# Kernel optimization log

Hardware: AMD Instinct MI355X
Metric: run time of the kernel (lower is better)

Reference implementation:

```python
import jax, jax.numpy as jnp
import numpy as np

NEG_SLOPE = 0.2

def gat_layer(x, src, dst, W, a_src, a_dst, num_nodes):
    """PyG-style GATConv. W:[F_in,H*C], a_src/a_dst:[H,C]. Returns [N,H,C]."""
    H, C = a_src.shape
    h = (x @ W).reshape(num_nodes, H, C)                      # [N,H,C]
    e_src = jnp.sum(h * a_src, axis=-1)                       # [N,H]
    e_dst = jnp.sum(h * a_dst, axis=-1)                       # [N,H]
    e = jax.nn.leaky_relu(e_src[src] + e_dst[dst], NEG_SLOPE) # [E,H]
    # segment softmax over incoming edges of each destination node
    m = jax.ops.segment_max(e, dst, num_segments=num_nodes)
    w = jnp.exp(e - m[dst])
    z = jax.ops.segment_sum(w, dst, num_segments=num_nodes)
    alpha = w / (z[dst] + 1e-16)                               # [E,H]
    msg = h[src] * alpha[:, :, None]                           # [E,H,C]
    return jax.ops.segment_sum(msg, dst, num_segments=num_nodes)


def setup_inputs() -> dict:
    key = jax.random.key(0)
    ks = jax.random.split(key, 16)
    N, E, F_IN, HID, A, G = 50000, 800000, 128, 128, 32, 64
    x = jax.random.normal(ks[0], (N, F_IN), dtype=jnp.float32)
    edge_index = jax.random.randint(ks[1], (2, E), 0, N, dtype=jnp.int32)
    batch = jnp.sort(jax.random.randint(ks[2], (N,), 0, G, dtype=jnp.int32))
    s = 0.1
    W1 = jax.random.normal(ks[3], (F_IN, 2 * HID), jnp.float32) * s
    a_src1 = jax.random.normal(ks[4], (2, HID), jnp.float32) * s
    a_dst1 = jax.random.normal(ks[5], (2, HID), jnp.float32) * s
    b1 = jnp.zeros((2 * HID,), jnp.float32)
    W2 = jax.random.normal(ks[6], (2 * HID, HID), jnp.float32) * s
    a_src2 = jax.random.normal(ks[7], (1, HID), jnp.float32) * s
    a_dst2 = jax.random.normal(ks[8], (1, HID), jnp.float32) * s
    b2 = jnp.zeros((HID,), jnp.float32)
    Wp = jax.random.normal(ks[9], (HID, A), jnp.float32) * s
    bp = jnp.zeros((A,), jnp.float32)
    Wv = jax.random.normal(ks[10], (HID, 1), jnp.float32) * s
    bv = jnp.zeros((1,), jnp.float32)
    return {"x": x, "edge_index": edge_index, "batch": batch,
            "W1": W1, "a_src1": a_src1, "a_dst1": a_dst1, "b1": b1,
            "W2": W2, "a_src2": a_src2, "a_dst2": a_dst2, "b2": b2,
            "Wp": Wp, "bp": bp, "Wv": Wv, "bv": bv}


def reference(x, edge_index, batch, W1, a_src1, a_dst1, b1,
              W2, a_src2, a_dst2, b2, Wp, bp, Wv, bv):
    N = x.shape[0]
    G = 64  # number of graphs in the batch
    # add self-loops (PyG GATConv default)
    loop = jnp.arange(N, dtype=edge_index.dtype)
    src = jnp.concatenate([edge_index[0], loop])
    dst = jnp.concatenate([edge_index[1], loop])
    # layer 1: heads=2, concat=True
    h1 = gat_layer(x, src, dst, W1, a_src1, a_dst1, N)        # [N,2,HID]
    h1 = jax.nn.elu(h1.reshape(N, -1) + b1)                   # [N,2*HID]
    # layer 2: heads=1, concat=False (mean over heads = identity for H=1)
    h2 = gat_layer(h1, src, dst, W2, a_src2, a_dst2, N)       # [N,1,HID]
    h2 = jax.nn.elu(h2.reshape(N, -1) + b2)                   # [N,HID]
    # global mean pool over graphs
    sums = jax.ops.segment_sum(h2, batch, num_segments=G)
    cnt = jax.ops.segment_sum(jnp.ones((N,), h2.dtype), batch, num_segments=G)
    x_pool = sums / jnp.maximum(cnt, 1.0)[:, None]            # [G,HID]
    policy_logits = x_pool @ Wp + bp                          # [G,A]
    state_value = x_pool @ Wv + bv                            # [G,1]
    return (policy_logits, state_value)
```

## Files before the change

kernel.cpp:

```cpp
#include <hip/hip_runtime.h>
#include <hip/hip_bf16.h>
#include <cstdint>


typedef __attribute__((ext_vector_type(8))) short bf16x8;
typedef __attribute__((ext_vector_type(4))) float f32x4;

#define NBLK_H 160
#define BSH 6
#define BMSK 63

__device__ __forceinline__ float wave_sum(float v) {
#pragma unroll
    for (int off = 32; off >= 1; off >>= 1) v += __shfl_xor(v, off, 64);
    return v;
}

__device__ __forceinline__ unsigned short f2bf(float f) {
    union { float f; uint32_t u; } c; c.f = f;
    uint32_t u = c.u;
    return (unsigned short)((u + 0x7fffu + ((u >> 16) & 1u)) >> 16);
}

__device__ __forceinline__ float bf2f(unsigned short u) {
    union { uint32_t u; float f; } c; c.u = ((uint32_t)u) << 16;
// ... 13 lines not shown
    int cg_ = rest;
    int quad = lane >> 4, lo = lane & 15;
    int col = colOff + cg_ * CPW + c * 16 + lo;
    unsigned short v[8];
#pragma unroll
    for (int j = 0; j < 8; ++j)
        v[j] = f2bf(W[(t * 32 + quad * 8 + j) * ldW + col]);
    ushort4* dst = (ushort4*)(Bsw + (size_t)tid * 8);
    ushort4 o0, o1;
    o0.x = v[0]; o0.y = v[1]; o0.z = v[2]; o0.w = v[3];
    o1.x = v[4]; o1.y = v[5]; o1.z = v[6]; o1.w = v[7];
    dst[0] = o0; dst[1] = o1;
}


__global__ __launch_bounds__(256) void init_kernel(
        const float* __restrict__ W1, const float* __restrict__ W2,
        const float* __restrict__ a_src1, const float* __restrict__ a_dst1,
        unsigned short* __restrict__ B1h0, unsigned short* __restrict__ B1h1,
        unsigned short* __restrict__ B2,
        float* __restrict__ v1s, float* __restrict__ v1d,
        int* __restrict__ zbase, int zn4, int ZB,
        const int* __restrict__ ei, int* __restrict__ hist,
        int E, int ET, int CHUNK, int NB) {
    __shared__ int bins[1024];
    int b = blockIdx.x;
    if (b < 8)        swizzle_body<128, 128>(W1, 256, 0,   B1h0, b * 256 + threadIdx.x);
    else if (b < 16)  swizzle_body<128, 128>(W1, 256, 128, B1h1, (b - 8) * 256 + threadIdx.x);
    else if (b < 32)  swizzle_body<256, 128>(W2, 128, 0,   B2, (b - 16) * 256 + threadIdx.x);
    else if (b == 32) {
        int t = threadIdx.x, h = t >> 7, k = t & 127;
        float vs = 0.f, vd = 0.f;
        for (int c = 0; c < 128; ++c) {
            float w = W1[k * 256 + h * 128 + c];
            vs += w * a_src1[h * 128 + c];
            vd += w * a_dst1[h * 128 + c];
        }
        v1s[h * 128 + k] = vs;
        v1d[h * 128 + k] = vd;
    } else if (b < 33 + ZB) {
        int i = (b - 33) * 256 + threadIdx.x;
        if (i < zn4) ((int4*)zbase)[i] = make_int4(0, 0, 0, 0);
    } else {
        const int blk = b - 33 - ZB;
        for (int t = threadIdx.x; t < NB; t += 256) bins[t] = 0;
        __syncthreads();
        const int start = blk * CHUNK, end = min(ET, start + CHUNK);
        for (int i = start + threadIdx.x; i < end; i += 256) {
            int dst = (i < E) ? ei[E + i] : (i - E);
            atomicAdd(&bins[dst >> BSH], 1);
        }
        __syncthreads();
        for (int t = threadIdx.x; t < NB; t += 256) hist[t * NBLK_H + blk] = bins[t];
    }
}


__global__ __launch_bounds__(256) void scan_attn1(
        int* __restrict__ hist, int* __restrict__ tsum, int M, int TILESH,
        const float* __restrict__ x, const float* __restrict__ v1s,
        const float* __restrict__ v1d, float* __restrict__ es1,
        float* __restrict__ ed1, unsigned short* __restrict__ xbf, int N) {
    __shared__ int buf[256];
    if ((int)blockIdx.x < TILESH) {
        const int t = threadIdx.x;
        const int base = blockIdx.x * 1024 + t * 4;
        int v[4]; int s = 0;
#pragma unroll
        for (int k = 0; k < 4; ++k) { v[k] = (base + k < M) ? hist[base + k] : 0; s += v[k]; }
        buf[t] = s;
        __syncthreads();
#pragma unroll
        for (int off = 1; off < 256; off <<= 1) {
            int xx = (t >= off) ? buf[t - off] : 0;
            __syncthreads();
            buf[t] += xx;
            __syncthreads();
        }
        int run = buf[t] - s;
#pragma unroll
        for (int k = 0; k < 4; ++k) {
            if (base + k < M) hist[base + k] = run;
            run += v[k];
        }
        if (t == 255) tsum[blockIdx.x] = buf[255];
        return;
    }
    int bid = blockIdx.x - TILESH;
    int wid = (bid * 256 + threadIdx.x) >> 6;
    int lane = threadIdx.x & 63;
    if (wid >= N) return;
    float2 xv = *(const float2*)(x + (size_t)wid * 128 + lane * 2);
    float p0s = xv.x * v1s[lane * 2] + xv.y * v1s[lane * 2 + 1];
    float p1s = xv.x * v1s[128 + lane * 2] + xv.y * v1s[128 + lane * 2 + 1];
    float p0d = xv.x * v1d[lane * 2] + xv.y * v1d[lane * 2 + 1];
    float p1d = xv.x * v1d[128 + lane * 2] + xv.y * v1d[128 + lane * 2 + 1];
    p0s = wave_sum(p0s); p1s = wave_sum(p1s);
    p0d = wave_sum(p0d); p1d = wave_sum(p1d);
    if (lane == 0) {
        es1[wid * 2] = p0s; es1[wid * 2 + 1] = p1s;
        ed1[wid * 2] = p0d; ed1[wid * 2 + 1] = p1d;
    }
    ushort2 o; o.x = f2bf(xv.x); o.y = f2bf(xv.y);
    *(ushort2*)(xbf + (size_t)wid * 128 + lane * 2) = o;
}


__global__ __launch_bounds__(256) void part_kernel(const int* __restrict__ ei,
                                                   const int* __restrict__ hist,
                                                   const int* __restrict__ tsum,
                                                   int* __restrict__ bsorted,
                                                   int* __restrict__ segbase,
                                                   int E, int ET, int CHUNK, int NB, int T) {
    __shared__ int sb[256];
    __shared__ int scur[1024];
    const int t = threadIdx.x;
    sb[t] = (t < T) ? tsum[t] : 0;
    __syncthreads();
#pragma unroll
    for (int off = 1; off < 256; off <<= 1) {
        int v = (t >= off) ? sb[t - off] : 0;
        __syncthreads();
        sb[t] += v;
        __syncthreads();
    }
    const int blk = blockIdx.x;
    for (int b = t; b < NB; b += 256) {
        int idx = b * NBLK_H + blk;
        int tile = idx >> 10;
        int v = hist[idx] + (tile ? sb[tile - 1] : 0);
        scur[b] = v;
        if (blk == 0) segbase[b] = v;
    }
    if (blk == 0 && t == 0) segbase[NB] = sb[T - 1];
    __syncthreads();
    const int start = blk * CHUNK, end = min(ET, start + CHUNK);
    for (int i = start + t; i < end; i += 256) {
        int dst = (i < E) ? ei[E + i] : (i - E);
        int src = (i < E) ? ei[i] : dst;
        int pos = atomicAdd(&scur[dst >> BSH], 1);
        bsorted[pos] = (src << BSH) | (dst & BMSK);
    }
}


__global__ __launch_bounds__(256) void bucket_kernel(const int* __restrict__ bsorted,
                                                     const int* __restrict__ segbase,
                                                     const float* __restrict__ es1,
                                                     const float* __restrict__ ed1,
                                                     int* __restrict__ csr_src,
                                                     float2* __restrict__ csr_alpha,
                                                     int* __restrict__ rowptr,
                                                     int N, int NB) {
    __shared__ int cnt[64], excl[64];
    __shared__ float z0[64], z1[64];
    __shared__ float2 edv[64];
    __shared__ int ebuf[3072];
    __shared__ float2 wbuf[3072];
    const int b = blockIdx.x;
    const int gbase = segbase[b], gend = segbase[b + 1];
    const int sz = gend - gbase;
    const int t = threadIdx.x;
    if (b == 0 && t == 0) rowptr[N] = segbase[NB];
    if (t < 64) {
        cnt[t] = 0; z0[t] = 0.f; z1[t] = 0.f;
        int dst = (b << BSH) + t;
        if (dst < N) edv[t] = *(const float2*)(ed1 + dst * 2);
        else edv[t] = make_float2(0.f, 0.f);
    }
    __syncthreads();
    const bool fits = (sz <= 3072);
    for (int i = t; i < sz; i += 256) {
        int p = bsorted[gbase + i];
        int s = p >> BSH, ld = p & BMSK;
        float2 esv = *(const float2*)(es1 + s * 2);
        float e0 = esv.x + edv[ld].x; e0 = (e0 > 0.f) ? e0 : 0.2f * e0;
        float e1 = esv.y + edv[ld].y; e1 = (e1 > 0.f) ? e1 : 0.2f * e1;
        float w0 = __expf(e0), w1 = __expf(e1);
        if (fits) { ebuf[i] = p; wbuf[i] = make_float2(w0, w1); }
        atomicAdd(&z0[ld], w0);
        atomicAdd(&z1[ld], w1);
        atomicAdd(&cnt[ld], 1);
    }
    __syncthreads();
    if (t < 64) excl[t] = cnt[t];
    __syncthreads();
    for (int off = 1; off < 64; off <<= 1) {
        int v = (t < 64 && t >= off) ? excl[t - off] : 0;
        __syncthreads();
        if (t < 64) excl[t] += v;
        __syncthreads();
    }
    if (t < 64) {
        int dst = (b << BSH) + t;
        if (dst < N) rowptr[dst] = gbase + excl[t] - cnt[t];
    }
    __syncthreads();
    if (t < 64) {
        cnt[t] = excl[t] - cnt[t];
        z0[t] = 1.f / (z0[t] + 1e-16f);
        z1[t] = 1.f / (z1[t] + 1e-16f);
    }
    __syncthreads();
    if (fits) {
        for (int i = t; i < sz; i += 256) {
            int p = ebuf[i]; float2 wv = wbuf[i];
            int ld = p & BMSK;
            int pos = atomicAdd(&cnt[ld], 1);
            csr_src[gbase + pos] = p >> BSH;
            csr_alpha[gbase + pos] = make_float2(wv.x * z0[ld], wv.y * z1[ld]);
        }
    } else {
        for (int i = t; i < sz; i += 256) {
            int p = bsorted[gbase + i];
            int s = p >> BSH, ld = p & BMSK;
            float2 esv = *(const float2*)(es1 + s * 2);
            float e0 = esv.x + edv[ld].x; e0 = (e0 > 0.f) ? e0 : 0.2f * e0;
            float e1 = esv.y + edv[ld].y; e1 = (e1 > 0.f) ? e1 : 0.2f * e1;
            float w0 = __expf(e0), w1 = __expf(e1);
            int pos = atomicAdd(&cnt[ld], 1);
            csr_src[gbase + pos] = s;
            csr_alpha[gbase + pos] = make_float2(w0 * z0[ld], w1 * z1[ld]);
        }
    }
}


#define ACC2(U_, WW_, P_, Q_) { float v_;                              \
    v_ = bf2f(U_.x); P_.x += WW_.x * v_; Q_.x += WW_.y * v_;           \
    v_ = bf2f(U_.y); P_.y += WW_.x * v_; Q_.y += WW_.y * v_;           \
    v_ = bf2f(U_.z); P_.z += WW_.x * v_; Q_.z += WW_.y * v_;           \
    v_ = bf2f(U_.w); P_.w += WW_.x * v_; Q_.w += WW_.y * v_; }

__global__ void gat_agg_x(const unsigned short* __restrict__ xbf,
                          const int* __restrict__ rowptr, const int* __restrict__ csr_src,
                          const float2* __restrict__ csr_alpha,
                          unsigned short* __restrict__ aggx, int N, int NPAD) {
// ... 178 lines not shown
            }
        }
    }
    __syncthreads();
    if (tid < 64) {
        int row = tid;
        int n = n0 + row;
        if (n < N) {
            es[n] = lds_ps[0][row] + lds_ps[1][row] + lds_ps[2][row] + lds_ps[3][row];
            ed[n] = lds_pd[0][row] + lds_pd[1][row] + lds_pd[2][row] + lds_pd[3][row];
        }
    }
}


__global__ void alpha2_kernel(const int* __restrict__ rowptr, const int* __restrict__ csr_src,
                              const float* __restrict__ es, const float* __restrict__ ed,
                              float* __restrict__ csr_a2, int N) {
    int wid = (blockIdx.x * blockDim.x + threadIdx.x) >> 6;
    int lane = threadIdx.x & 63;
    if (wid >= N) return;
    const int rs = rowptr[wid], re = rowptr[wid + 1];
    const float edn = ed[wid];
    float z = 0.f;
    for (int i = rs; i < re; i += 64) {
        int cnt = min(re - i, 64);
        if (lane < cnt) {
            int s = csr_src[i + lane];
            float e = es[s] + edn;
            e = (e > 0.f) ? e : 0.2f * e;
            float w = __expf(e);
            csr_a2[i + lane] = w;
            z += w;
        }
    }
    z = wave_sum(z);
    const float rz = 1.f / (z + 1e-16f);
    for (int i = rs + lane; i < re; i += 64) csr_a2[i] *= rz;
}


#define ACC1(U_, W_, P_) {                                   \
    P_.x += W_ * bf2f(U_.x); P_.y += W_ * bf2f(U_.y);        \
    P_.z += W_ * bf2f(U_.z); P_.w += W_ * bf2f(U_.w); }

__global__ void gat_agg_h1(const unsigned short* __restrict__ Hpre,
                           const int* __restrict__ rowptr, const int* __restrict__ csr_src,
                           const float* __restrict__ csr_a2,
                           const float* __restrict__ bias, unsigned short* __restrict__ out,
                           int N) {
    __shared__ int   s_lds[4][2][32];
    __shared__ float a_lds[4][2][32];
    const int wave = threadIdx.x >> 6, lane = threadIdx.x & 63;
    const int g = lane >> 5, c = lane & 31;
    const int node = (blockIdx.x * 4 + wave) * 2 + g;
    if (node >= N) return;
    const int rs = rowptr[node], re = rowptr[node + 1];
    float4 p = {0.f, 0.f, 0.f, 0.f};
    for (int i = rs; i < re; i += 32) {
        const int cnt = min(re - i, 32);
        if (c < cnt) {
            s_lds[wave][g][c] = csr_src[i + c];
            a_lds[wave][g][c] = csr_a2[i + c];
        }
        int k = 0;
        for (; k + 7 < cnt; k += 8) {
            int s0 = s_lds[wave][g][k + 0], s1 = s_lds[wave][g][k + 1];
            int s2 = s_lds[wave][g][k + 2], s3 = s_lds[wave][g][k + 3];
            int s4 = s_lds[wave][g][k + 4], s5 = s_lds[wave][g][k + 5];
            int s6 = s_lds[wave][g][k + 6], s7 = s_lds[wave][g][k + 7];
            float a0 = a_lds[wave][g][k + 0], a1 = a_lds[wave][g][k + 1];
            float a2 = a_lds[wave][g][k + 2], a3 = a_lds[wave][g][k + 3];
            float a4 = a_lds[wave][g][k + 4], a5 = a_lds[wave][g][k + 5];
            float a6 = a_lds[wave][g][k + 6], a7 = a_lds[wave][g][k + 7];
            ushort4 u0 = *(const ushort4*)(Hpre + (size_t)s0 * 128 + c * 4);
            ushort4 u1 = *(const ushort4*)(Hpre + (size_t)s1 * 128 + c * 4);
            ushort4 u2 = *(const ushort4*)(Hpre + (size_t)s2 * 128 + c * 4);
            ushort4 u3 = *(const ushort4*)(Hpre + (size_t)s3 * 128 + c * 4);
            ushort4 u4 = *(const ushort4*)(Hpre + (size_t)s4 * 128 + c * 4);
            ushort4 u5 = *(const ushort4*)(Hpre + (size_t)s5 * 128 + c * 4);
            ushort4 u6 = *(const ushort4*)(Hpre + (size_t)s6 * 128 + c * 4);
            ushort4 u7 = *(const ushort4*)(Hpre + (size_t)s7 * 128 + c * 4);
            ACC1(u0, a0, p);
            ACC1(u1, a1, p);
            ACC1(u2, a2, p);
            ACC1(u3, a3, p);
            ACC1(u4, a4, p);
            ACC1(u5, a5, p);
            ACC1(u6, a6, p);
            ACC1(u7, a7, p);
        }
        for (; k < cnt; ++k) {
            int s0 = s_lds[wave][g][k];
            float a0 = a_lds[wave][g][k];
            ushort4 u0 = *(const ushort4*)(Hpre + (size_t)s0 * 128 + c * 4);
            ACC1(u0, a0, p);
        }
    }
    float4 bv = ((const float4*)bias)[c];
    float ox = p.x + bv.x, oy = p.y + bv.y, oz = p.z + bv.z, ow = p.w + bv.w;
    ox = (ox > 0.f) ? ox : __expf(ox) - 1.f;
    oy = (oy > 0.f) ? oy : __expf(oy) - 1.f;
    oz = (oz > 0.f) ? oz : __expf(oz) - 1.f;
    ow = (ow > 0.f) ? ow : __expf(ow) - 1.f;
    ushort4 o;
    o.x = f2bf(ox); o.y = f2bf(oy); o.z = f2bf(oz); o.w = f2bf(ow);
    *(ushort4*)(out + (size_t)node * 128 + c * 4) = o;
}


#define PCHUNK 256

__global__ __launch_bounds__(256) void pool_partial(const unsigned short* __restrict__ h2,
                                                    const int* __restrict__ batch,
                                                    float* __restrict__ xsum,
                                                    int* __restrict__ cnt, int N) {
    const int base = blockIdx.x * PCHUNK;
    const int rg = threadIdx.x >> 6;
    const int c2 = threadIdx.x & 63;
    float ax = 0.f, ay = 0.f;
    int gcur = -1, run = 0;
    for (int r = rg; r < PCHUNK; r += 4) {
        int i = base + r;
        if (i >= N) break;
        int g = batch[i];
        if (g != gcur) {
            if (gcur >= 0) {
                atomicAdd(&xsum[gcur * 128 + c2 * 2 + 0], ax);
                atomicAdd(&xsum[gcur * 128 + c2 * 2 + 1], ay);
                if (c2 == 0) atomicAdd(&cnt[gcur], run);
            }
            gcur = g; ax = 0.f; ay = 0.f; run = 0;
        }
        ushort2 u = *(const ushort2*)(h2 + (size_t)i * 128 + c2 * 2);
        ax += bf2f(u.x); ay += bf2f(u.y);
        run += 1;
    }
    if (gcur >= 0) {
        atomicAdd(&xsum[gcur * 128 + c2 * 2 + 0], ax);
        atomicAdd(&xsum[gcur * 128 + c2 * 2 + 1], ay);
        if (c2 == 0) atomicAdd(&cnt[gcur], run);
    }
}


__global__ void head_kernel(const float* __restrict__ xsum, const int* __restrict__ cnt,
                            const float* __restrict__ Wp, const float* __restrict__ bp,
                            const float* __restrict__ Wv, const float* __restrict__ bv,
                            float* __restrict__ out) {
    int g = blockIdx.x, t = threadIdx.x;
    __shared__ float p[128];
    float inv = 1.f / fmaxf((float)cnt[g], 1.f);
    p[t] = xsum[g * 128 + t] * inv;
    p[t + 64] = xsum[g * 128 + t + 64] * inv;
    __syncthreads();
    if (t < 32) {
        float acc = bp[t];
        for (int k = 0; k < 128; ++k) acc += p[k] * Wp[k * 32 + t];
        out[g * 32 + t] = acc;
    } else if (t == 32) {
        float acc = bv[0];
        for (int k = 0; k < 128; ++k) acc += p[k] * Wv[k];
        out[64 * 32 + g] = acc;
    }
}


extern "C" void kernel_launch(void* const* d_in, const int* in_sizes, int n_in,
                              void* d_out, int out_size, void* d_ws, size_t ws_size,
                              hipStream_t stream) {
    const float* x      = (const float*)d_in[0];
    const int*   ei     = (const int*)d_in[1];
    const int*   batch  = (const int*)d_in[2];
    const float* W1     = (const float*)d_in[3];
    const float* a_src1 = (const float*)d_in[4];
    const float* a_dst1 = (const float*)d_in[5];
    const float* b1     = (const float*)d_in[6];
    const float* W2     = (const float*)d_in[7];
    const float* a_src2 = (const float*)d_in[8];
    const float* a_dst2 = (const float*)d_in[9];
    const float* b2     = (const float*)d_in[10];
    const float* Wp     = (const float*)d_in[11];
    const float* bp     = (const float*)d_in[12];
    const float* Wv     = (const float*)d_in[13];
    const float* bv     = (const float*)d_in[14];

    const int N  = in_sizes[0] / 128;
    const int E  = in_sizes[1] / 2;
    const int ET = E + N;
    const int NPAD = ((N + 63) / 64) * 64;
    const int NBLK = NPAD / 64;
    const int PBLK = (N + PCHUNK - 1) / PCHUNK;
    const int NB = (N + 63) >> BSH;
    const int CHUNK = (ET + NBLK_H - 1) / NBLK_H;
    const int M = NB * NBLK_H;
    const int TILESH = (M + 1023) / 1024;
    const int AB = (N + 3) / 4;
    const int GB = (N + 7) / 8;

    char* ws = (char*)d_ws;
    size_t off = 0;
    auto alloc = [&](size_t bytes) -> void* {
        void* p = ws + off;
        off = (off + bytes + 255) & ~(size_t)255;
        return p;
    };
    unsigned short* xbf   = (unsigned short*)alloc((size_t)NPAD * 128 * 2);
    unsigned short* aggx  = (unsigned short*)alloc((size_t)2 * NPAD * 128 * 2);
    unsigned short* h2pre = (unsigned short*)alloc((size_t)NPAD * 128 * 2);
    unsigned short* h2bf  = (unsigned short*)alloc((size_t)N * 128 * 2);
    unsigned short* w1h0  = (unsigned short*)alloc((size_t)128 * 128 * 2);
    unsigned short* w1h1  = (unsigned short*)alloc((size_t)128 * 128 * 2);
    unsigned short* w2sw  = (unsigned short*)alloc((size_t)256 * 128 * 2);
    float* v1s = (float*)alloc(256 * 4);
    float* v1d = (float*)alloc(256 * 4);
    float* es1 = (float*)alloc((size_t)N * 2 * 4);
    float* ed1 = (float*)alloc((size_t)N * 2 * 4);
    float* es2 = (float*)alloc((size_t)N * 4);
    float* ed2 = (float*)alloc((size_t)N * 4);
    const int ZINTS = 64 * 128 + 64;
    int*   zbase  = (int*)alloc(((size_t)ZINTS + 8) * 4);
    float* xsum   = (float*)zbase;
    int*   cnt    = (int*)(xsum + 64 * 128);
    int*    rowptr    = (int*)alloc((size_t)(N + 1) * 4);
    int*    hist      = (int*)alloc((size_t)M * 4);
    int*    segbase   = (int*)alloc((size_t)(NB + 1) * 4);
    int*    bsorted   = (int*)alloc((size_t)ET * 4);
    int*    csrsrc    = (int*)alloc((size_t)ET * 4);
    float2* csralpha  = (float2*)alloc((size_t)ET * 8);
    float*  csra2     = (float*)alloc((size_t)ET * 4);
    int*    tsum      = (int*)alloc(256 * 4);
    const int zn4 = (ZINTS + 3) / 4;
    const int ZB = (zn4 + 255) / 256;

    init_kernel<<<33 + ZB + NBLK_H, 256, 0, stream>>>(W1, W2, a_src1, a_dst1,
                                                      w1h0, w1h1, w2sw, v1s, v1d,
                                                      zbase, zn4, ZB,
                                                      ei, hist, E, ET, CHUNK, NB);
    scan_attn1<<<TILESH + AB, 256, 0, stream>>>(hist, tsum, M, TILESH,
                                                x, v1s, v1d, es1, ed1, xbf, N);
    part_kernel<<<NBLK_H, 256, 0, stream>>>(ei, hist, tsum, bsorted, segbase,
                                            E, ET, CHUNK, NB, TILESH);
    bucket_kernel<<<NB, 256, 0, stream>>>(bsorted, segbase, es1, ed1,
                                          csrsrc, csralpha, rowptr, N, NB);
    gat_agg_x<<<GB, 256, 0, stream>>>(xbf, rowptr, csrsrc, csralpha, aggx, N, NPAD);
    gemm12_fused<<<NBLK, 256, 0, stream>>>(aggx, w1h0, w1h1, w2sw, b1,
                                           a_src2, a_dst2, es2, ed2, h2pre, N, NPAD);
    alpha2_kernel<<<AB, 256, 0, stream>>>(rowptr, csrsrc, es2, ed2, csra2, N);
    gat_agg_h1<<<GB, 256, 0, stream>>>(h2pre, rowptr, csrsrc, csra2, b2, h2bf, N);
    pool_partial<<<PBLK, 256, 0, stream>>>(h2bf, batch, xsum, cnt, N);
    head_kernel<<<64, 64, 0, stream>>>(xsum, cnt, Wp, bp, Wv, bv, (float*)d_out);
}
```

Measured before the change: 304.9 us.

## Merge front and tail stages into persistent cooperative kernels with grid syncs

Replaces the four preprocessing kernels (init, scan/attn1, partition, bucket) with one cooperative persistent kernel that runs them as phases separated by grid-wide syncs. The tail stages (alpha2, layer-2 aggregation, pooling, head) become a second cooperative kernel of the same kind, which also drops the separate csra2 buffer by computing alpha inline. The partition chunk count goes from 160 to 256, and bucket_kernel loses its shared-memory edge buffer, so it reads bsorted twice. The aim is to cut launch gaps and tail idle time between the many small kernels. The cost is grid-sync overhead, and occupancy is limited to what a co-resident grid allows. Separate per-phase launches remain as a fallback.

```diff
diff --git a/kernel.cpp b/kernel.cpp
--- a/kernel.cpp
+++ b/kernel.cpp
@@ -1,14 +1,18 @@
 #include <hip/hip_runtime.h>
 #include <hip/hip_bf16.h>
+#include <hip/hip_cooperative_groups.h>
 #include <cstdint>
 
+
+namespace cg = cooperative_groups;
 
 typedef __attribute__((ext_vector_type(8))) short bf16x8;
 typedef __attribute__((ext_vector_type(4))) float f32x4;
 
-#define NBLK_H 160
 #define BSH 6
 #define BMSK 63
+#define NCH_F 256
+#define PCHUNK 256
 
 __device__ __forceinline__ float wave_sum(float v) {
 #pragma unroll
@@ -52,7 +56,8 @@
 }
 
 
-__global__ __launch_bounds__(256) void init_kernel(
+__global__ __launch_bounds__(256, 4) void front_kernel(
+        int phase,
         const float* __restrict__ W1, const float* __restrict__ W2,
         const float* __restrict__ a_src1, const float* __restrict__ a_dst1,
         unsigned short* __restrict__ B1h0, unsigned short* __restrict__ B1h1,
@@ -60,205 +65,200 @@
         float* __restrict__ v1s, float* __restrict__ v1d,
         int* __restrict__ zbase, int zn4, int ZB,
         const int* __restrict__ ei, int* __restrict__ hist,
-        int E, int ET, int CHUNK, int NB) {
-    __shared__ int bins[1024];
-    int b = blockIdx.x;
-    if (b < 8)        swizzle_body<128, 128>(W1, 256, 0,   B1h0, b * 256 + threadIdx.x);
-    else if (b < 16)  swizzle_body<128, 128>(W1, 256, 128, B1h1, (b - 8) * 256 + threadIdx.x);
-    else if (b < 32)  swizzle_body<256, 128>(W2, 128, 0,   B2, (b - 16) * 256 + threadIdx.x);
-    else if (b == 32) {
-        int t = threadIdx.x, h = t >> 7, k = t & 127;
-        float vs = 0.f, vd = 0.f;
-        for (int c = 0; c < 128; ++c) {
-            float w = W1[k * 256 + h * 128 + c];
-            vs += w * a_src1[h * 128 + c];
-            vd += w * a_dst1[h * 128 + c];
-        }
-        v1s[h * 128 + k] = vs;
-        v1d[h * 128 + k] = vd;
-    } else if (b < 33 + ZB) {
-        int i = (b - 33) * 256 + threadIdx.x;
-        if (i < zn4) ((int4*)zbase)[i] = make_int4(0, 0, 0, 0);
-    } else {
-        const int blk = b - 33 - ZB;
-        for (int t = threadIdx.x; t < NB; t += 256) bins[t] = 0;
-        __syncthreads();
-        const int start = blk * CHUNK, end = min(ET, start + CHUNK);
-        for (int i = start + threadIdx.x; i < end; i += 256) {
-            int dst = (i < E) ? ei[E + i] : (i - E);
-            atomicAdd(&bins[dst >> BSH], 1);
-        }
-        __syncthreads();
-        for (int t = threadIdx.x; t < NB; t += 256) hist[t * NBLK_H + blk] = bins[t];
-    }
-}
-
-
-__global__ __launch_bounds__(256) void scan_attn1(
-        int* __restrict__ hist, int* __restrict__ tsum, int M, int TILESH,
-        const float* __restrict__ x, const float* __restrict__ v1s,
-        const float* __restrict__ v1d, float* __restrict__ es1,
-        float* __restrict__ ed1, unsigned short* __restrict__ xbf, int N) {
-    __shared__ int buf[256];
-    if ((int)blockIdx.x < TILESH) {
-        const int t = threadIdx.x;
-        const int base = blockIdx.x * 1024 + t * 4;
-        int v[4]; int s = 0;
-#pragma unroll
-        for (int k = 0; k < 4; ++k) { v[k] = (base + k < M) ? hist[base + k] : 0; s += v[k]; }
-        buf[t] = s;
-        __syncthreads();
-#pragma unroll
-        for (int off = 1; off < 256; off <<= 1) {
-            int xx = (t >= off) ? buf[t - off] : 0;
-            __syncthreads();
-            buf[t] += xx;
-            __syncthreads();
-        }
-        int run = buf[t] - s;
-#pragma unroll
-        for (int k = 0; k < 4; ++k) {
-            if (base + k < M) hist[base + k] = run;
-            run += v[k];
-        }
-        if (t == 255) tsum[blockIdx.x] = buf[255];
-        return;
-    }
-    int bid = blockIdx.x - TILESH;
-    int wid = (bid * 256 + threadIdx.x) >> 6;
-    int lane = threadIdx.x & 63;
-    if (wid >= N) return;
-    float2 xv = *(const float2*)(x + (size_t)wid * 128 + lane * 2);
-    float p0s = xv.x * v1s[lane * 2] + xv.y * v1s[lane * 2 + 1];
-    float p1s = xv.x * v1s[128 + lane * 2] + xv.y * v1s[128 + lane * 2 + 1];
-    float p0d = xv.x * v1d[lane * 2] + xv.y * v1d[lane * 2 + 1];
-    float p1d = xv.x * v1d[128 + lane * 2] + xv.y * v1d[128 + lane * 2 + 1];
-    p0s = wave_sum(p0s); p1s = wave_sum(p1s);
-    p0d = wave_sum(p0d); p1d = wave_sum(p1d);
-    if (lane == 0) {
-        es1[wid * 2] = p0s; es1[wid * 2 + 1] = p1s;
-        ed1[wid * 2] = p0d; ed1[wid * 2 + 1] = p1d;
-    }
-    ushort2 o; o.x = f2bf(xv.x); o.y = f2bf(xv.y);
-    *(ushort2*)(xbf + (size_t)wid * 128 + lane * 2) = o;
-}
-
-
-__global__ __launch_bounds__(256) void part_kernel(const int* __restrict__ ei,
-                                                   const int* __restrict__ hist,
-                                                   const int* __restrict__ tsum,
-                                                   int* __restrict__ bsorted,
-                                                   int* __restrict__ segbase,
-                                                   int E, int ET, int CHUNK, int NB, int T) {
-    __shared__ int sb[256];
-    __shared__ int scur[1024];
+        int* __restrict__ tsum, int* __restrict__ bsorted, int* __restrict__ segbase,
+        const float* __restrict__ x, float* __restrict__ es1, float* __restrict__ ed1,
+        unsigned short* __restrict__ xbf,
+        int* __restrict__ csr_src, float2* __restrict__ csr_alpha,
+        int* __restrict__ rowptr,
+        int E, int ET, int N, int NB) {
+    __shared__ char smraw[8192] __attribute__((aligned(16)));
+    const bool all = (phase < 0);
     const int t = threadIdx.x;
-    sb[t] = (t < T) ? tsum[t] : 0;
-    __syncthreads();
-#pragma unroll
-    for (int off = 1; off < 256; off <<= 1) {
-        int v = (t >= off) ? sb[t - off] : 0;
-        __syncthreads();
-        sb[t] += v;
-        __syncthreads();
-    }
-    const int blk = blockIdx.x;
-    for (int b = t; b < NB; b += 256) {
-        int idx = b * NBLK_H + blk;
-        int tile = idx >> 10;
-        int v = hist[idx] + (tile ? sb[tile - 1] : 0);
-        scur[b] = v;
-        if (blk == 0) segbase[b] = v;
-    }
-    if (blk == 0 && t == 0) segbase[NB] = sb[T - 1];
-    __syncthreads();
-    const int start = blk * CHUNK, end = min(ET, start + CHUNK);
-    for (int i = start + t; i < end; i += 256) {
-        int dst = (i < E) ? ei[E + i] : (i - E);
-        int src = (i < E) ? ei[i] : dst;
-        int pos = atomicAdd(&scur[dst >> BSH], 1);
-        bsorted[pos] = (src << BSH) | (dst & BMSK);
-    }
-}
-
-
-__global__ __launch_bounds__(256) void bucket_kernel(const int* __restrict__ bsorted,
-                                                     const int* __restrict__ segbase,
-                                                     const float* __restrict__ es1,
-                                                     const float* __restrict__ ed1,
-                                                     int* __restrict__ csr_src,
-                                                     float2* __restrict__ csr_alpha,
-                                                     int* __restrict__ rowptr,
-                                                     int N, int NB) {
-    __shared__ int cnt[64], excl[64];
-    __shared__ float z0[64], z1[64];
-    __shared__ float2 edv[64];
-    __shared__ int ebuf[3072];
-    __shared__ float2 wbuf[3072];
-    const int b = blockIdx.x;
-    const int gbase = segbase[b], gend = segbase[b + 1];
-    const int sz = gend - gbase;
-    const int t = threadIdx.x;
-    if (b == 0 && t == 0) rowptr[N] = segbase[NB];
-    if (t < 64) {
-        cnt[t] = 0; z0[t] = 0.f; z1[t] = 0.f;
-        int dst = (b << BSH) + t;
-        if (dst < N) edv[t] = *(const float2*)(ed1 + dst * 2);
-        else edv[t] = make_float2(0.f, 0.f);
-    }
-    __syncthreads();
-    const bool fits = (sz <= 3072);
-    for (int i = t; i < sz; i += 256) {
-        int p = bsorted[gbase + i];
-        int s = p >> BSH, ld = p & BMSK;
-        float2 esv = *(const float2*)(es1 + s * 2);
-        float e0 = esv.x + edv[ld].x; e0 = (e0 > 0.f) ? e0 : 0.2f * e0;
-        float e1 = esv.y + edv[ld].y; e1 = (e1 > 0.f) ? e1 : 0.2f * e1;
-        float w0 = __expf(e0), w1 = __expf(e1);
-        if (fits) { ebuf[i] = p; wbuf[i] = make_float2(w0, w1); }
-        atomicAdd(&z0[ld], w0);
-        atomicAdd(&z1[ld], w1);
-        atomicAdd(&cnt[ld], 1);
-    }
-    __syncthreads();
-    if (t < 64) excl[t] = cnt[t];
-    __syncthreads();
-    for (int off = 1; off < 64; off <<= 1) {
-        int v = (t < 64 && t >= off) ? excl[t - off] : 0;
-        __syncthreads();
-        if (t < 64) excl[t] += v;
-        __syncthreads();
-    }
-    if (t < 64) {
-        int dst = (b << BSH) + t;
-        if (dst < N) rowptr[dst] = gbase + excl[t] - cnt[t];
-    }
-    __syncthreads();
-    if (t < 64) {
-        cnt[t] = excl[t] - cnt[t];
-        z0[t] = 1.f / (z0[t] + 1e-16f);
-        z1[t] = 1.f / (z1[t] + 1e-16f);
-    }
-    __syncthreads();
-    if (fits) {
-        for (int i = t; i < sz; i += 256) {
-            int p = ebuf[i]; float2 wv = wbuf[i];
-            int ld = p & BMSK;
-            int pos = atomicAdd(&cnt[ld], 1);
-            csr_src[gbase + pos] = p >> BSH;
-            csr_alpha[gbase + pos] = make_float2(wv.x * z0[ld], wv.y * z1[ld]);
-        }
-    } else {
-        for (int i = t; i < sz; i += 256) {
-            int p = bsorted[gbase + i];
-            int s = p >> BSH, ld = p & BMSK;
-            float2 esv = *(const float2*)(es1 + s * 2);
-            float e0 = esv.x + edv[ld].x; e0 = (e0 > 0.f) ? e0 : 0.2f * e0;
-            float e1 = esv.y + edv[ld].y; e1 = (e1 > 0.f) ? e1 : 0.2f * e1;
-            float w0 = __expf(e0), w1 = __expf(e1);
-            int pos = atomicAdd(&cnt[ld], 1);
-            csr_src[gbase + pos] = s;
-            csr_alpha[gbase + pos] = make_float2(w0 * z0[ld], w1 * z1[ld]);
+    const int G = gridDim.x;
+    const int CHUNK = (ET + NCH_F - 1) / NCH_F;
+    const int M = NB * NCH_F;
+    const int TILES = (M + 1023) >> 10;
+    const int TOT0 = 33 + ZB + NCH_F;
+
+    if (all || phase == 0) {
+        for (int bb = blockIdx.x; bb < TOT0; bb += G) {
+            if (bb < 8)       swizzle_body<128, 128>(W1, 256, 0,   B1h0, bb * 256 + t);
+            else if (bb < 16) swizzle_body<128, 128>(W1, 256, 128, B1h1, (bb - 8) * 256 + t);
+            else if (bb < 32) swizzle_body<256, 128>(W2, 128, 0,   B2, (bb - 16) * 256 + t);
+            else if (bb == 32) {
+                int h = t >> 7, k = t & 127;
+                float vs = 0.f, vd = 0.f;
+                for (int c = 0; c < 128; ++c) {
+                    float w = W1[k * 256 + h * 128 + c];
+                    vs += w * a_src1[h * 128 + c];
+                    vd += w * a_dst1[h * 128 + c];
+                }
+                v1s[h * 128 + k] = vs;
+                v1d[h * 128 + k] = vd;
+            } else if (bb < 33 + ZB) {
+                int i = (bb - 33) * 256 + t;
+                if (i < zn4) ((int4*)zbase)[i] = make_int4(0, 0, 0, 0);
+            } else {
+                int* bins = (int*)smraw;
+                const int blk = bb - 33 - ZB;
+                for (int i = t; i < NB; i += 256) bins[i] = 0;
+                __syncthreads();
+                const int start = blk * CHUNK, end = min(ET, start + CHUNK);
+                for (int i = start + t; i < end; i += 256) {
+                    int dst = (i < E) ? ei[E + i] : (i - E);
+                    atomicAdd(&bins[dst >> BSH], 1);
+                }
+                __syncthreads();
+                for (int i = t; i < NB; i += 256) hist[i * NCH_F + blk] = bins[i];
+                __syncthreads();
+            }
+        }
+    }
+    if (all) cg::this_grid().sync();
+
+    if (all || phase == 1) {
+        for (int tt = blockIdx.x; tt < TILES; tt += G) {
+            int* buf = (int*)smraw;
+            const int base = tt * 1024 + t * 4;
+            int v[4]; int s = 0;
+#pragma unroll
+            for (int k = 0; k < 4; ++k) { v[k] = (base + k < M) ? hist[base + k] : 0; s += v[k]; }
+            buf[t] = s;
+            __syncthreads();
+#pragma unroll
+            for (int off = 1; off < 256; off <<= 1) {
+                int xx = (t >= off) ? buf[t - off] : 0;
+                __syncthreads();
+                buf[t] += xx;
+                __syncthreads();
+            }
+            int run = buf[t] - s;
+#pragma unroll
+            for (int k = 0; k < 4; ++k) {
+                if (base + k < M) hist[base + k] = run;
+                run += v[k];
+            }
+            if (t == 255) tsum[tt] = buf[255];
+            __syncthreads();
+        }
+        {
+            const int AB = (N + 3) / 4;
+            const int lane = t & 63;
+            for (int gq = blockIdx.x; gq < AB; gq += G) {
+                int wid = gq * 4 + (t >> 6);
+                if (wid < N) {
+                    float2 xv = *(const float2*)(x + (size_t)wid * 128 + lane * 2);
+                    float p0s = xv.x * v1s[lane * 2] + xv.y * v1s[lane * 2 + 1];
+                    float p1s = xv.x * v1s[128 + lane * 2] + xv.y * v1s[128 + lane * 2 + 1];
+                    float p0d = xv.x * v1d[lane * 2] + xv.y * v1d[lane * 2 + 1];
+                    float p1d = xv.x * v1d[128 + lane * 2] + xv.y * v1d[128 + lane * 2 + 1];
+                    p0s = wave_sum(p0s); p1s = wave_sum(p1s);
+                    p0d = wave_sum(p0d); p1d = wave_sum(p1d);
+                    if (lane == 0) {
+                        es1[wid * 2] = p0s; es1[wid * 2 + 1] = p1s;
+                        ed1[wid * 2] = p0d; ed1[wid * 2 + 1] = p1d;
+                    }
+                    ushort2 o; o.x = f2bf(xv.x); o.y = f2bf(xv.y);
+                    *(ushort2*)(xbf + (size_t)wid * 128 + lane * 2) = o;
+                }
+            }
+        }
+    }
+    if (all) cg::this_grid().sync();
+
+    if (all || phase == 2) {
+        for (int ch = blockIdx.x; ch < NCH_F; ch += G) {
+            int* sb = (int*)smraw;
+            int* scur = (int*)(smraw + 1024);
+            sb[t] = (t < TILES) ? tsum[t] : 0;
+            __syncthreads();
+#pragma unroll
+            for (int off = 1; off < 256; off <<= 1) {
+                int v = (t >= off) ? sb[t - off] : 0;
+                __syncthreads();
+                sb[t] += v;
+                __syncthreads();
+            }
+            for (int bb = t; bb < NB; bb += 256) {
+                int idx = bb * NCH_F + ch;
+                int tile = idx >> 10;
+                int v = hist[idx] + (tile ? sb[tile - 1] : 0);
+                scur[bb] = v;
+                if (ch == 0) segbase[bb] = v;
+            }
+            if (ch == 0 && t == 0) segbase[NB] = sb[TILES - 1];
+            __syncthreads();
+            const int start = ch * CHUNK, end = min(ET, start + CHUNK);
+            for (int i = start + t; i < end; i += 256) {
+                int dst = (i < E) ? ei[E + i] : (i - E);
+                int src = (i < E) ? ei[i] : dst;
+                int pos = atomicAdd(&scur[dst >> BSH], 1);
+                bsorted[pos] = (src << BSH) | (dst & BMSK);
+            }
+            __syncthreads();
+        }
+    }
+    if (all) cg::this_grid().sync();
+
+    if (all || phase == 3) {
+        for (int b = blockIdx.x; b < NB; b += G) {
+            int* cnt = (int*)smraw;
+            int* excl = cnt + 64;
+            float* z0 = (float*)(excl + 64);
+            float* z1 = z0 + 64;
+            float* e0v = z1 + 64;
+            float* e1v = e0v + 64;
+            const int gbase = segbase[b], gend = segbase[b + 1];
+            const int sz = gend - gbase;
+            if (b == 0 && t == 0) rowptr[N] = segbase[NB];
+            if (t < 64) {
+                cnt[t] = 0; z0[t] = 0.f; z1[t] = 0.f;
+                int dst = (b << BSH) + t;
+                if (dst < N) { e0v[t] = ed1[dst * 2]; e1v[t] = ed1[dst * 2 + 1]; }
+                else { e0v[t] = 0.f; e1v[t] = 0.f; }
+            }
+            __syncthreads();
+            for (int i = t; i < sz; i += 256) {
+                int p = bsorted[gbase + i];
+                int s = p >> BSH, ld = p & BMSK;
+                float2 esv = *(const float2*)(es1 + s * 2);
+                float e0 = esv.x + e0v[ld]; e0 = (e0 > 0.f) ? e0 : 0.2f * e0;
+                float e1 = esv.y + e1v[ld]; e1 = (e1 > 0.f) ? e1 : 0.2f * e1;
+                atomicAdd(&z0[ld], __expf(e0));
+                atomicAdd(&z1[ld], __expf(e1));
+                atomicAdd(&cnt[ld], 1);
+            }
+            __syncthreads();
+            if (t < 64) excl[t] = cnt[t];
+            __syncthreads();
+            for (int off = 1; off < 64; off <<= 1) {
+                int v = (t < 64 && t >= off) ? excl[t - off] : 0;
+                __syncthreads();
+                if (t < 64) excl[t] += v;
+                __syncthreads();
+            }
+            if (t < 64) {
+                int dst = (b << BSH) + t;
+                if (dst < N) rowptr[dst] = gbase + excl[t] - cnt[t];
+            }
+            __syncthreads();
+            if (t < 64) {
+                cnt[t] = excl[t] - cnt[t];
+                z0[t] = 1.f / (z0[t] + 1e-16f);
+                z1[t] = 1.f / (z1[t] + 1e-16f);
+            }
+            __syncthreads();
+            for (int i = t; i < sz; i += 256) {
+                int p = bsorted[gbase + i];
+                int s = p >> BSH, ld = p & BMSK;
+                float2 esv = *(const float2*)(es1 + s * 2);
+                float e0 = esv.x + e0v[ld]; e0 = (e0 > 0.f) ? e0 : 0.2f * e0;
+                float e1 = esv.y + e1v[ld]; e1 = (e1 > 0.f) ? e1 : 0.2f * e1;
+                int pos = atomicAdd(&cnt[ld], 1);
+                csr_src[gbase + pos] = s;
+                csr_alpha[gbase + pos] = make_float2(__expf(e0) * z0[ld], __expf(e1) * z1[ld]);
+            }
+            __syncthreads();
         }
     }
 }
@@ -467,154 +467,155 @@
 }
 
 
-__global__ void alpha2_kernel(const int* __restrict__ rowptr, const int* __restrict__ csr_src,
-                              const float* __restrict__ es, const float* __restrict__ ed,
-                              float* __restrict__ csr_a2, int N) {
-    int wid = (blockIdx.x * blockDim.x + threadIdx.x) >> 6;
-    int lane = threadIdx.x & 63;
-    if (wid >= N) return;
-    const int rs = rowptr[wid], re = rowptr[wid + 1];
-    const float edn = ed[wid];
-    float z = 0.f;
-    for (int i = rs; i < re; i += 64) {
-        int cnt = min(re - i, 64);
-        if (lane < cnt) {
-            int s = csr_src[i + lane];
-            float e = es[s] + edn;
-            e = (e > 0.f) ? e : 0.2f * e;
-            float w = __expf(e);
-            csr_a2[i + lane] = w;
-            z += w;
-        }
-    }
-    z = wave_sum(z);
-    const float rz = 1.f / (z + 1e-16f);
-    for (int i = rs + lane; i < re; i += 64) csr_a2[i] *= rz;
-}
-
-
 #define ACC1(U_, W_, P_) {                                   \
     P_.x += W_ * bf2f(U_.x); P_.y += W_ * bf2f(U_.y);        \
     P_.z += W_ * bf2f(U_.z); P_.w += W_ * bf2f(U_.w); }
 
-__global__ void gat_agg_h1(const unsigned short* __restrict__ Hpre,
-                           const int* __restrict__ rowptr, const int* __restrict__ csr_src,
-                           const float* __restrict__ csr_a2,
-                           const float* __restrict__ bias, unsigned short* __restrict__ out,
-                           int N) {
+__global__ __launch_bounds__(256, 4) void tail_kernel(
+        int phase,
+        const unsigned short* __restrict__ Hpre,
+        const int* __restrict__ rowptr, const int* __restrict__ csr_src,
+        const float* __restrict__ es, const float* __restrict__ ed,
+        const float* __restrict__ b2, unsigned short* __restrict__ h2bf,
+        const int* __restrict__ batch, float* __restrict__ xsum, int* __restrict__ cntg,
+        const float* __restrict__ Wp, const float* __restrict__ bp,
+        const float* __restrict__ Wv, const float* __restrict__ bv,
+        float* __restrict__ out, int N) {
     __shared__ int   s_lds[4][2][32];
     __shared__ float a_lds[4][2][32];
-    const int wave = threadIdx.x >> 6, lane = threadIdx.x & 63;
+    __shared__ float hp[128];
+    const bool all = (phase < 0);
+    const int t = threadIdx.x;
+    const int G = gridDim.x;
+    const int wave = t >> 6, lane = t & 63;
     const int g = lane >> 5, c = lane & 31;
-    const int node = (blockIdx.x * 4 + wave) * 2 + g;
-    if (node >= N) return;
-    const int rs = rowptr[node], re = rowptr[node + 1];
-    float4 p = {0.f, 0.f, 0.f, 0.f};
-    for (int i = rs; i < re; i += 32) {
-        const int cnt = min(re - i, 32);
-        if (c < cnt) {
-            s_lds[wave][g][c] = csr_src[i + c];
-            a_lds[wave][g][c] = csr_a2[i + c];
-        }
-        int k = 0;
-        for (; k + 7 < cnt; k += 8) {
-            int s0 = s_lds[wave][g][k + 0], s1 = s_lds[wave][g][k + 1];
-            int s2 = s_lds[wave][g][k + 2], s3 = s_lds[wave][g][k + 3];
-            int s4 = s_lds[wave][g][k + 4], s5 = s_lds[wave][g][k + 5];
-            int s6 = s_lds[wave][g][k + 6], s7 = s_lds[wave][g][k + 7];
-            float a0 = a_lds[wave][g][k + 0], a1 = a_lds[wave][g][k + 1];
-            float a2 = a_lds[wave][g][k + 2], a3 = a_lds[wave][g][k + 3];
-            float a4 = a_lds[wave][g][k + 4], a5 = a_lds[wave][g][k + 5];
-            float a6 = a_lds[wave][g][k + 6], a7 = a_lds[wave][g][k + 7];
-            ushort4 u0 = *(const ushort4*)(Hpre + (size_t)s0 * 128 + c * 4);
-            ushort4 u1 = *(const ushort4*)(Hpre + (size_t)s1 * 128 + c * 4);
-            ushort4 u2 = *(const ushort4*)(Hpre + (size_t)s2 * 128 + c * 4);
-            ushort4 u3 = *(const ushort4*)(Hpre + (size_t)s3 * 128 + c * 4);
-            ushort4 u4 = *(const ushort4*)(Hpre + (size_t)s4 * 128 + c * 4);
-            ushort4 u5 = *(const ushort4*)(Hpre + (size_t)s5 * 128 + c * 4);
-            ushort4 u6 = *(const ushort4*)(Hpre + (size_t)s6 * 128 + c * 4);
-            ushort4 u7 = *(const ushort4*)(Hpre + (size_t)s7 * 128 + c * 4);
-            ACC1(u0, a0, p);
-            ACC1(u1, a1, p);
-            ACC1(u2, a2, p);
-            ACC1(u3, a3, p);
-            ACC1(u4, a4, p);
-            ACC1(u5, a5, p);
-            ACC1(u6, a6, p);
-            ACC1(u7, a7, p);
-        }
-        for (; k < cnt; ++k) {
-            int s0 = s_lds[wave][g][k];
-            float a0 = a_lds[wave][g][k];
-            ushort4 u0 = *(const ushort4*)(Hpre + (size_t)s0 * 128 + c * 4);
-            ACC1(u0, a0, p);
-        }
-    }
-    float4 bv = ((const float4*)bias)[c];
-    float ox = p.x + bv.x, oy = p.y + bv.y, oz = p.z + bv.z, ow = p.w + bv.w;
-    ox = (ox > 0.f) ? ox : __expf(ox) - 1.f;
-    oy = (oy > 0.f) ? oy : __expf(oy) - 1.f;
-    oz = (oz > 0.f) ? oz : __expf(oz) - 1.f;
-    ow = (ow > 0.f) ? ow : __expf(ow) - 1.f;
-    ushort4 o;
-    o.x = f2bf(ox); o.y = f2bf(oy); o.z = f2bf(oz); o.w = f2bf(ow);
-    *(ushort4*)(out + (size_t)node * 128 + c * 4) = o;
-}
-
-
-#define PCHUNK 256
-
-__global__ __launch_bounds__(256) void pool_partial(const unsigned short* __restrict__ h2,
-                                                    const int* __restrict__ batch,
-                                                    float* __restrict__ xsum,
-                                                    int* __restrict__ cnt, int N) {
-    const int base = blockIdx.x * PCHUNK;
-    const int rg = threadIdx.x >> 6;
-    const int c2 = threadIdx.x & 63;
-    float ax = 0.f, ay = 0.f;
-    int gcur = -1, run = 0;
-    for (int r = rg; r < PCHUNK; r += 4) {
-        int i = base + r;
-        if (i >= N) break;
-        int g = batch[i];
-        if (g != gcur) {
+
+    if (all || phase == 0) {
+        const int GBn = (N + 7) / 8;
+        for (int blk = blockIdx.x; blk < GBn; blk += G) {
+            const int node = (blk * 4 + wave) * 2 + g;
+            if (node < N) {
+                const int rs = rowptr[node], re = rowptr[node + 1];
+                const float edn = ed[node];
+                float z = 0.f;
+                for (int i = rs; i < re; i += 32) {
+                    if (c < min(re - i, 32)) {
+                        int s = csr_src[i + c];
+                        float e = es[s] + edn;
+                        e = (e > 0.f) ? e : 0.2f * e;
+                        z += __expf(e);
+                    }
+                }
+#pragma unroll
+                for (int off = 16; off >= 1; off >>= 1) z += __shfl_xor(z, off, 64);
+                const float rz = 1.f / (z + 1e-16f);
+                float4 p = {0.f, 0.f, 0.f, 0.f};
+                for (int i = rs; i < re; i += 32) {
+                    const int cnt = min(re - i, 32);
+                    if (c < cnt) {
+                        int s = csr_src[i + c];
+                        float e = es[s] + edn;
+                        e = (e > 0.f) ? e : 0.2f * e;
+                        s_lds[wave][g][c] = s;
+                        a_lds[wave][g][c] = __expf(e) * rz;
+                    }
+                    int k = 0;
+                    for (; k + 7 < cnt; k += 8) {
+                        int s0 = s_lds[wave][g][k + 0], s1 = s_lds[wave][g][k + 1];
+                        int s2 = s_lds[wave][g][k + 2], s3 = s_lds[wave][g][k + 3];
+                        int s4 = s_lds[wave][g][k + 4], s5 = s_lds[wave][g][k + 5];
+                        int s6 = s_lds[wave][g][k + 6], s7 = s_lds[wave][g][k + 7];
+                        float a0 = a_lds[wave][g][k + 0], a1 = a_lds[wave][g][k + 1];
+                        float a2 = a_lds[wave][g][k + 2], a3 = a_lds[wave][g][k + 3];
+                        float a4 = a_lds[wave][g][k + 4], a5 = a_lds[wave][g][k + 5];
+                        float a6 = a_lds[wave][g][k + 6], a7 = a_lds[wave][g][k + 7];
+                        ushort4 u0 = *(const ushort4*)(Hpre + (size_t)s0 * 128 + c * 4);
+                        ushort4 u1 = *(const ushort4*)(Hpre + (size_t)s1 * 128 + c * 4);
+                        ushort4 u2 = *(const ushort4*)(Hpre + (size_t)s2 * 128 + c * 4);
+                        ushort4 u3 = *(const ushort4*)(Hpre + (size_t)s3 * 128 + c * 4);
+                        ushort4 u4 = *(const ushort4*)(Hpre + (size_t)s4 * 128 + c * 4);
+                        ushort4 u5 = *(const ushort4*)(Hpre + (size_t)s5 * 128 + c * 4);
+                        ushort4 u6 = *(const ushort4*)(Hpre + (size_t)s6 * 128 + c * 4);
+                        ushort4 u7 = *(const ushort4*)(Hpre + (size_t)s7 * 128 + c * 4);
+                        ACC1(u0, a0, p);
+                        ACC1(u1, a1, p);
+                        ACC1(u2, a2, p);
+                        ACC1(u3, a3, p);
+                        ACC1(u4, a4, p);
+                        ACC1(u5, a5, p);
+                        ACC1(u6, a6, p);
+                        ACC1(u7, a7, p);
+                    }
+                    for (; k < cnt; ++k) {
+                        int s0 = s_lds[wave][g][k];
+                        float a0 = a_lds[wave][g][k];
+                        ushort4 u0 = *(const ushort4*)(Hpre + (size_t)s0 * 128 + c * 4);
+                        ACC1(u0, a0, p);
+                    }
+                }
+                float4 bv4 = ((const float4*)b2)[c];
+                float ox = p.x + bv4.x, oy = p.y + bv4.y, oz = p.z + bv4.z, ow = p.w + bv4.w;
+                ox = (ox > 0.f) ? ox : __expf(ox) - 1.f;
+                oy = (oy > 0.f) ? oy : __expf(oy) - 1.f;
+                oz = (oz > 0.f) ? oz : __expf(oz) - 1.f;
+                ow = (ow > 0.f) ? ow : __expf(ow) - 1.f;
+                ushort4 o;
+                o.x = f2bf(ox); o.y = f2bf(oy); o.z = f2bf(oz); o.w = f2bf(ow);
+                *(ushort4*)(h2bf + (size_t)node * 128 + c * 4) = o;
+            }
+        }
+    }
+    if (all) cg::this_grid().sync();
+
+    if (all || phase == 1) {
+        const int PBLK = (N + PCHUNK - 1) / PCHUNK;
+        const int rg = t >> 6;
+        const int c2 = t & 63;
+        for (int blk = blockIdx.x; blk < PBLK; blk += G) {
+            const int base = blk * PCHUNK;
+            float ax = 0.f, ay = 0.f;
+            int gcur = -1, run = 0;
+            for (int r = rg; r < PCHUNK; r += 4) {
+                int i = base + r;
+                if (i >= N) break;
+                int gg = batch[i];
+                if (gg != gcur) {
+                    if (gcur >= 0) {
+                        atomicAdd(&xsum[gcur * 128 + c2 * 2 + 0], ax);
+                        atomicAdd(&xsum[gcur * 128 + c2 * 2 + 1], ay);
+                        if (c2 == 0) atomicAdd(&cntg[gcur], run);
+                    }
+                    gcur = gg; ax = 0.f; ay = 0.f; run = 0;
+                }
+                ushort2 u = *(const ushort2*)(h2bf + (size_t)i * 128 + c2 * 2);
+                ax += bf2f(u.x); ay += bf2f(u.y);
+                run += 1;
+            }
             if (gcur >= 0) {
                 atomicAdd(&xsum[gcur * 128 + c2 * 2 + 0], ax);
                 atomicAdd(&xsum[gcur * 128 + c2 * 2 + 1], ay);
-                if (c2 == 0) atomicAdd(&cnt[gcur], run);
-            }
-            gcur = g; ax = 0.f; ay = 0.f; run = 0;
-        }
-        ushort2 u = *(const ushort2*)(h2 + (size_t)i * 128 + c2 * 2);
-        ax += bf2f(u.x); ay += bf2f(u.y);
-        run += 1;
-    }
-    if (gcur >= 0) {
-        atomicAdd(&xsum[gcur * 128 + c2 * 2 + 0], ax);
-        atomicAdd(&xsum[gcur * 128 + c2 * 2 + 1], ay);
-        if (c2 == 0) atomicAdd(&cnt[gcur], run);
-    }
-}
-
-
-__global__ void head_kernel(const float* __restrict__ xsum, const int* __restrict__ cnt,
-                            const float* __restrict__ Wp, const float* __restrict__ bp,
-                            const float* __restrict__ Wv, const float* __restrict__ bv,
-                            float* __restrict__ out) {
-    int g = blockIdx.x, t = threadIdx.x;
-    __shared__ float p[128];
-    float inv = 1.f / fmaxf((float)cnt[g], 1.f);
-    p[t] = xsum[g * 128 + t] * inv;
-    p[t + 64] = xsum[g * 128 + t + 64] * inv;
-    __syncthreads();
-    if (t < 32) {
-        float acc = bp[t];
-        for (int k = 0; k < 128; ++k) acc += p[k] * Wp[k * 32 + t];
-        out[g * 32 + t] = acc;
-    } else if (t == 32) {
-        float acc = bv[0];
-        for (int k = 0; k < 128; ++k) acc += p[k] * Wv[k];
-        out[64 * 32 + g] = acc;
+                if (c2 == 0) atomicAdd(&cntg[gcur], run);
+            }
+        }
+    }
+    if (all) cg::this_grid().sync();
+
+    if (all || phase == 2) {
+        for (int gg = blockIdx.x; gg < 64; gg += G) {
+            float inv = 1.f / fmaxf((float)cntg[gg], 1.f);
+            if (t < 128) hp[t] = xsum[gg * 128 + t] * inv;
+            __syncthreads();
+            if (t < 32) {
+                float acc = bp[t];
+                for (int k = 0; k < 128; ++k) acc += hp[k] * Wp[k * 32 + t];
+                out[gg * 32 + t] = acc;
+            } else if (t == 32) {
+                float acc = bv[0];
+                for (int k = 0; k < 128; ++k) acc += hp[k] * Wv[k];
+                out[64 * 32 + gg] = acc;
+            }
+            __syncthreads();
+        }
     }
 }
 
@@ -638,18 +639,34 @@
     const float* Wv     = (const float*)d_in[13];
     const float* bv     = (const float*)d_in[14];
 
-    const int N  = in_sizes[0] / 128;
-    const int E  = in_sizes[1] / 2;
-    const int ET = E + N;
+    int N  = in_sizes[0] / 128;
+    int E  = in_sizes[1] / 2;
+    int ET = E + N;
     const int NPAD = ((N + 63) / 64) * 64;
     const int NBLK = NPAD / 64;
+    int NB = (N + 63) >> BSH;
+    const int M = NB * NCH_F;
+    const int GB = (N + 7) / 8;
     const int PBLK = (N + PCHUNK - 1) / PCHUNK;
-    const int NB = (N + 63) >> BSH;
-    const int CHUNK = (ET + NBLK_H - 1) / NBLK_H;
-    const int M = NB * NBLK_H;
+    const int AB = (N + 3) / 4;
     const int TILESH = (M + 1023) / 1024;
-    const int AB = (N + 3) / 4;
-    const int GB = (N + 7) / 8;
+
+    static int nCU = 0, occF = 0, occT = 0;
+    if (nCU == 0) {
+        hipDeviceProp_t prop;
+        if (hipGetDeviceProperties(&prop, 0) == hipSuccess && prop.multiProcessorCount > 0)
+            nCU = prop.multiProcessorCount;
+        else
+            nCU = 256;
+        if (hipOccupancyMaxActiveBlocksPerMultiprocessor(&occF, (const void*)front_kernel,
+                                                         256, 0) != hipSuccess || occF <= 0)
+            occF = 1;
+        if (hipOccupancyMaxActiveBlocksPerMultiprocessor(&occT, (const void*)tail_kernel,
+                                                         256, 0) != hipSuccess || occT <= 0)
+            occT = 1;
+    }
+    int G1 = occF * nCU; if (G1 > 2048) G1 = 2048;
+    int G2 = occT * nCU; if (G2 > 2048) G2 = 2048;
 
     char* ws = (char*)d_ws;
     size_t off = 0;
@@ -674,33 +691,69 @@
     const int ZINTS = 64 * 128 + 64;
     int*   zbase  = (int*)alloc(((size_t)ZINTS + 8) * 4);
     float* xsum   = (float*)zbase;
-    int*   cnt    = (int*)(xsum + 64 * 128);
+    int*   cntg   = (int*)(xsum + 64 * 128);
     int*    rowptr    = (int*)alloc((size_t)(N + 1) * 4);
     int*    hist      = (int*)alloc((size_t)M * 4);
     int*    segbase   = (int*)alloc((size_t)(NB + 1) * 4);
     int*    bsorted   = (int*)alloc((size_t)ET * 4);
     int*    csrsrc    = (int*)alloc((size_t)ET * 4);
     float2* csralpha  = (float2*)alloc((size_t)ET * 8);
-    float*  csra2     = (float*)alloc((size_t)ET * 4);
     int*    tsum      = (int*)alloc(256 * 4);
-    const int zn4 = (ZINTS + 3) / 4;
-    const int ZB = (zn4 + 255) / 256;
-
-    init_kernel<<<33 + ZB + NBLK_H, 256, 0, stream>>>(W1, W2, a_src1, a_dst1,
-                                                      w1h0, w1h1, w2sw, v1s, v1d,
-                                                      zbase, zn4, ZB,
-                                                      ei, hist, E, ET, CHUNK, NB);
-    scan_attn1<<<TILESH + AB, 256, 0, stream>>>(hist, tsum, M, TILESH,
-                                                x, v1s, v1d, es1, ed1, xbf, N);
-    part_kernel<<<NBLK_H, 256, 0, stream>>>(ei, hist, tsum, bsorted, segbase,
-                                            E, ET, CHUNK, NB, TILESH);
-    bucket_kernel<<<NB, 256, 0, stream>>>(bsorted, segbase, es1, ed1,
-                                          csrsrc, csralpha, rowptr, N, NB);
+    int zn4 = (ZINTS + 3) / 4;
+    int ZB = (zn4 + 255) / 256;
+    const int TOT0 = 33 + ZB + NCH_F;
+    float* outp = (float*)d_out;
+
+    {
+        int allphase = -1;
+        void* fargs[] = {
+            (void*)&allphase,
+            (void*)&W1, (void*)&W2, (void*)&a_src1, (void*)&a_dst1,
+            (void*)&w1h0, (void*)&w1h1, (void*)&w2sw,
+            (void*)&v1s, (void*)&v1d, (void*)&zbase, (void*)&zn4, (void*)&ZB,
+            (void*)&ei, (void*)&hist, (void*)&tsum, (void*)&bsorted, (void*)&segbase,
+            (void*)&x, (void*)&es1, (void*)&ed1, (void*)&xbf,
+            (void*)&csrsrc, (void*)&csralpha, (void*)&rowptr,
+            (void*)&E, (void*)&ET, (void*)&N, (void*)&NB };
+        hipError_t e1 = hipLaunchCooperativeKernel((void*)front_kernel, dim3(G1), dim3(256),
+                                                   fargs, 0, stream);
+        if (e1 != hipSuccess) {
+            front_kernel<<<TOT0, 256, 0, stream>>>(0, W1, W2, a_src1, a_dst1, w1h0, w1h1,
+                w2sw, v1s, v1d, zbase, zn4, ZB, ei, hist, tsum, bsorted, segbase,
+                x, es1, ed1, xbf, csrsrc, csralpha, rowptr, E, ET, N, NB);
+            int g1p = (TILESH > AB) ? TILESH : AB;
+            front_kernel<<<g1p, 256, 0, stream>>>(1, W1, W2, a_src1, a_dst1, w1h0, w1h1,
+                w2sw, v1s, v1d, zbase, zn4, ZB, ei, hist, tsum, bsorted, segbase,
+                x, es1, ed1, xbf, csrsrc, csralpha, rowptr, E, ET, N, NB);
+            front_kernel<<<NCH_F, 256, 0, stream>>>(2, W1, W2, a_src1, a_dst1, w1h0, w1h1,
+                w2sw, v1s, v1d, zbase, zn4, ZB, ei, hist, tsum, bsorted, segbase,
+                x, es1, ed1, xbf, csrsrc, csralpha, rowptr, E, ET, N, NB);
+            front_kernel<<<NB, 256, 0, stream>>>(3, W1, W2, a_src1, a_dst1, w1h0, w1h1,
+                w2sw, v1s, v1d, zbase, zn4, ZB, ei, hist, tsum, bsorted, segbase,
+                x, es1, ed1, xbf, csrsrc, csralpha, rowptr, E, ET, N, NB);
+        }
+    }
     gat_agg_x<<<GB, 256, 0, stream>>>(xbf, rowptr, csrsrc, csralpha, aggx, N, NPAD);
     gemm12_fused<<<NBLK, 256, 0, stream>>>(aggx, w1h0, w1h1, w2sw, b1,
                                            a_src2, a_dst2, es2, ed2, h2pre, N, NPAD);
-    alpha2_kernel<<<AB, 256, 0, stream>>>(rowptr, csrsrc, es2, ed2, csra2, N);
-    gat_agg_h1<<<GB, 256, 0, stream>>>(h2pre, rowptr, csrsrc, csra2, b2, h2bf, N);
-    pool_partial<<<PBLK, 256, 0, stream>>>(h2bf, batch, xsum, cnt, N);
-    head_kernel<<<64, 64, 0, stream>>>(xsum, cnt, Wp, bp, Wv, bv, (float*)d_out);
-}
+    {
+        int allphase = -1;
+        void* targs[] = {
+            (void*)&allphase,
+            (void*)&h2pre, (void*)&rowptr, (void*)&csrsrc,
+            (void*)&es2, (void*)&ed2, (void*)&b2, (void*)&h2bf,
+            (void*)&batch, (void*)&xsum, (void*)&cntg,
+            (void*)&Wp, (void*)&bp, (void*)&Wv, (void*)&bv,
+            (void*)&outp, (void*)&N };
+        hipError_t e2 = hipLaunchCooperativeKernel((void*)tail_kernel, dim3(G2), dim3(256),
+                                                   targs, 0, stream);
+        if (e2 != hipSuccess) {
+            tail_kernel<<<GB, 256, 0, stream>>>(0, h2pre, rowptr, csrsrc, es2, ed2, b2,
+                h2bf, batch, xsum, cntg, Wp, bp, Wv, bv, outp, N);
+            tail_kernel<<<PBLK, 256, 0, stream>>>(1, h2pre, rowptr, csrsrc, es2, ed2, b2,
+                h2bf, batch, xsum, cntg, Wp, bp, Wv, bv, outp, N);
+            tail_kernel<<<64, 256, 0, stream>>>(2, h2pre, rowptr, csrsrc, es2, ed2, b2,
+                h2bf, batch, xsum, cntg, Wp, bp, Wv, bv, outp, N);
+        }
+    }
+}
```

After: 800.0 us. 162% more time.
